# Kernel optimization log

Hardware: AMD Instinct MI355X
Metric: run time of the kernel (lower is better)

The kernel has to match this reference:

```python
import jax, jax.numpy as jnp
import numpy as np

N = 50000      # nodes
E = 800000     # edges (avg degree 16)
D_IN = 64
D_OUT = 64


def setup_inputs() -> dict:
    key = jax.random.key(0)
    k1, k2, k3 = jax.random.split(key, 3)
    x = jax.random.normal(k1, (N, D_IN), dtype=jnp.float32)
    edge_index = jax.random.randint(k2, (2, E), 0, N, dtype=jnp.int32)
    W = jax.random.normal(k3, (D_OUT, D_IN), dtype=jnp.float32) * 0.05
    b = jnp.zeros((D_OUT,), dtype=jnp.float32)
    prelu_a = jnp.full((1,), 0.25, dtype=jnp.float32)  # nn.PReLU() default
    return {"x": x, "edge_index": edge_index, "W": W, "b": b, "prelu_a": prelu_a}


def reference(x, edge_index, W, b, prelu_a):
    # GCNConv (PyG, normalize=True, add_self_loops=True) + PReLU.
    # Dropout is identity at inference and omitted.
    n = x.shape[0]
    row, col = edge_index[0], edge_index[1]
    loop = jnp.arange(n, dtype=edge_index.dtype)
    row = jnp.concatenate([row, loop])  # [E+N] source nodes
    col = jnp.concatenate([col, loop])  # [E+N] target nodes

    # Symmetric degree normalization: deg over targets (edge weight = 1).
    ones = jnp.ones(row.shape[0], dtype=x.dtype)
    deg = jax.ops.segment_sum(ones, col, num_segments=n)          # [N]
    dinv = jnp.where(deg > 0, jax.lax.rsqrt(deg), 0.0)            # deg^{-1/2}
    norm = dinv[row] * dinv[col]                                  # [E+N]

    h = x @ W.T                                                   # [N, D_OUT]
    msg = h[row] * norm[:, None]                                  # gather + scale
    out = jax.ops.segment_sum(msg, col, num_segments=n) + b       # scatter-add

    # PReLU with a single shared slope parameter
    return jnp.where(out >= 0, out, prelu_a * out)
```

## Files before the change

kernel.cpp:

```cpp
#include <hip/hip_runtime.h>
#include <hip/hip_bf16.h>

#define D 64
#define CAP 64
#define GROUPS 8
#define ZERO_BLOCKS 49

__global__ void __launch_bounds__(256) gemm_zero_kernel(
    const float* __restrict__ x, const float* __restrict__ W,
    __hip_bfloat16* __restrict__ h, int4* __restrict__ cnt4, int nzero4, int n)
{
    if (blockIdx.x < ZERO_BLOCKS) {
        int i = blockIdx.x * 256 + threadIdx.x;
        if (i < nzero4) cnt4[i] = make_int4(0, 0, 0, 0);
    }

    __shared__ float Ws[D * 65];
    __shared__ float xs[4][D];

    int tid = threadIdx.x;
    #pragma unroll
    for (int k = 0; k < 16; ++k) {
        int idx = tid + k * 256;
        int o = idx >> 6, i = idx & 63;
        Ws[o * 65 + i] = W[idx];
    }

    int ln = tid >> 6;
    int o  = tid & 63;
    int node = blockIdx.x * 4 + ln;
    if (node < n) {
        xs[ln][o] = x[node * D + o];
    }
    __syncthreads();

    if (node >= n) return;

    float sum = 0.0f;
    #pragma unroll
    for (int i = 0; i < D; ++i) {
        sum += xs[ln][i] * Ws[o * 65 + i];
    }
    h[(size_t)node * D + o] = __float2bfloat16(sum);
}

__global__ void __launch_bounds__(256) fill_kernel(
    const int* __restrict__ row, const int* __restrict__ col,
    const int4* __restrict__ row4, const int4* __restrict__ col4,
    int* __restrict__ cnt, unsigned short* __restrict__ srcs,
    int* __restrict__ ovf_cnt, int2* __restrict__ ovf, int E, int E4, int n)
{
    int g   = blockIdx.x & (GROUPS - 1);
    int bg  = blockIdx.x >> 3;
    int bpg = gridDim.x >> 3;
    int npg = (n + GROUPS - 1) / GROUPS;
    int lo  = g * npg;
    int hi  = lo + npg < n ? lo + npg : n;
    int stride = bpg * 256;

    for (int i = bg * 256 + threadIdx.x; i < E4; i += stride) {
        int4 cc = col4[i];
        int4 rr = row4[i];
        #pragma unroll
        for (int j = 0; j < 4; ++j) {
            int c = (j == 0) ? cc.x : (j == 1) ? cc.y : (j == 2) ? cc.z : cc.w;
            int r = (j == 0) ? rr.x : (j == 1) ? rr.y : (j == 2) ? rr.z : rr.w;
            if (c >= lo && c < hi) {
                int slot = atomicAdd(&cnt[c], 1);
                if (slot < CAP) {
                    srcs[(size_t)c * CAP + slot] = (unsigned short)r;
                } else {
                    int oi = atomicAdd(ovf_cnt, 1);
                    ovf[oi] = make_int2(r, c);
                }
            }
        }
    }
    for (int e = E4 * 4 + bg * 256 + threadIdx.x; e < E; e += stride) {
        int c = col[e];
        if (c >= lo && c < hi) {
            int r = row[e];
            int slot = atomicAdd(&cnt[c], 1);
            if (slot < CAP) {
                srcs[(size_t)c * CAP + slot] = (unsigned short)r;
            } else {
                int oi = atomicAdd(ovf_cnt, 1);
                ovf[oi] = make_int2(r, c);
            }
        }
    }
}

__global__ void __launch_bounds__(256) gather_kernel(
    const int* __restrict__ cnt, const unsigned short* __restrict__ srcs,
    const __hip_bfloat16* __restrict__ h,
    const float* __restrict__ b, const float* __restrict__ prelu_a,
    const int* __restrict__ ovf_cnt, const int2* __restrict__ ovf,
    float* __restrict__ out, int n)
{
    int wave = (blockIdx.x * blockDim.x + threadIdx.x) >> 6;
    int lane = threadIdx.x & 63;
    if (wave >= n) return;
    int c = wave;

    int deg = cnt[c];
    int m = deg < CAP ? deg : CAP;
    float dc = rsqrtf((float)deg + 1.0f);

    int   s  = 0;
    float wl = 0.0f;
    if (lane < m) {
        s  = (int)srcs[(size_t)c * CAP + lane];
        wl = rsqrtf((float)cnt[s] + 1.0f) * dc;
    }

    float acc = __bfloat162float(h[(size_t)c * D + lane]) * dc * dc + b[lane];

    int m8 = (m + 7) & ~7;
    for (int k = 0; k < m8; k += 8) {
        int   ss[8];
        float ww[8];
        #pragma unroll
        for (int j = 0; j < 8; ++j) {
            ss[j] = __shfl(s,  k + j);
            ww[j] = __shfl(wl, k + j);
        }
        float vv[8];
        #pragma unroll
        for (int j = 0; j < 8; ++j) {
            vv[j] = __bfloat162float(h[(size_t)ss[j] * D + lane]);
        }
        #pragma unroll
        for (int j = 0; j < 8; ++j) {
            acc += vv[j] * ww[j];
        }
    }

    int nov = *ovf_cnt;
    for (int i = 0; i < nov; ++i) {
        int2 rc = ovf[i];
        if (rc.y == c) {
            acc += __bfloat162float(h[(size_t)rc.x * D + lane]) *
                   rsqrtf((float)cnt[rc.x] + 1.0f) * dc;
        }
    }

    float al = prelu_a[0];
    out[(size_t)c * D + lane] = acc >= 0.0f ? acc : al * acc;
}

extern "C" void kernel_launch(void* const* d_in, const int* in_sizes, int n_in,
                              void* d_out, int out_size, void* d_ws, size_t ws_size,
                              hipStream_t stream) {
    const float* x       = (const float*)d_in[0];
    const int*   eidx    = (const int*)d_in[1];
    const float* W       = (const float*)d_in[2];
    const float* b       = (const float*)d_in[3];
    const float* prelu_a = (const float*)d_in[4];

    const int E = in_sizes[1] / 2;
    const int n = in_sizes[0] / D;
    const int* row = eidx;
    const int* col = eidx + E;

    float* out = (float*)d_out;

    int E4 = 0;
    if ((E % 4) == 0 &&
        ((uintptr_t)row % 16) == 0 && ((uintptr_t)col % 16) == 0) {
        E4 = E / 4;
    }

    int*   cnt     = (int*)d_ws;
    int*   ovf_cnt = cnt + n;
    int2*  ovf     = (int2*)(cnt + n + 2);
    __hip_bfloat16* h = (__hip_bfloat16*)(ovf + E);
    unsigned short* srcs = (unsigned short*)(h + (size_t)n * D);

    int nzero4 = (n + 1 + 3) / 4;

    gemm_zero_kernel<<<(n + 3) / 4, 256, 0, stream>>>(
        x, W, h, (int4*)cnt, nzero4, n);

    fill_kernel<<<2048, 256, 0, stream>>>(
        row, col, (const int4*)row, (const int4*)col,
        cnt, srcs, ovf_cnt, ovf, E, E4, n);

    gather_kernel<<<(n * 64 + 255) / 256, 256, 0, stream>>>(
        cnt, srcs, h, b, prelu_a, ovf_cnt, ovf, out, n);
}
```

Before: 100.2 us.

## Split feature dimension into two 32-channel halves with separate gather passes

The GEMM now writes h in a column-split layout: two contiguous [n,32] bf16 halves. The gather runs twice, once per half. Each half-wave handles alternate neighbors over 32 channels, and the two partial sums are combined with a cross-half shuffle. The goal is to shrink the working set of each gather pass so the random neighbor reads hit L2/MALL more often. The cost is a second launch and repeated reads of the CSR indices and degrees.

New measurement: 112.2 us. 1.12x slower.

```diff
diff --git a/kernel.cpp b/kernel.cpp
--- a/kernel.cpp
+++ b/kernel.cpp
@@ -41,7 +41,8 @@
     for (int i = 0; i < D; ++i) {
         sum += xs[ln][i] * Ws[o * 65 + i];
     }
-    h[(size_t)node * D + o] = __float2bfloat16(sum);
+    h[(size_t)(o >> 5) * n * 32 + (size_t)node * 32 + (o & 31)] =
+        __float2bfloat16(sum);
 }
 
 __global__ void __launch_bounds__(256) fill_kernel(
@@ -91,17 +92,19 @@
     }
 }
 
-__global__ void __launch_bounds__(256) gather_kernel(
+__global__ void __launch_bounds__(256) gather_half_kernel(
     const int* __restrict__ cnt, const unsigned short* __restrict__ srcs,
-    const __hip_bfloat16* __restrict__ h,
+    const __hip_bfloat16* __restrict__ hh,
     const float* __restrict__ b, const float* __restrict__ prelu_a,
     const int* __restrict__ ovf_cnt, const int2* __restrict__ ovf,
-    float* __restrict__ out, int n)
+    float* __restrict__ out, int n, int half)
 {
     int wave = (blockIdx.x * blockDim.x + threadIdx.x) >> 6;
     int lane = threadIdx.x & 63;
     if (wave >= n) return;
-    int c = wave;
+    int c  = wave;
+    int p  = lane >> 5;
+    int ch = lane & 31;
 
     int deg = cnt[c];
     int m = deg < CAP ? deg : CAP;
@@ -114,39 +117,45 @@
         wl = rsqrtf((float)cnt[s] + 1.0f) * dc;
     }
 
-    float acc = __bfloat162float(h[(size_t)c * D + lane]) * dc * dc + b[lane];
-
+    float acc = 0.0f;
     int m8 = (m + 7) & ~7;
     for (int k = 0; k < m8; k += 8) {
-        int   ss[8];
-        float ww[8];
-        #pragma unroll
-        for (int j = 0; j < 8; ++j) {
-            ss[j] = __shfl(s,  k + j);
-            ww[j] = __shfl(wl, k + j);
-        }
-        float vv[8];
-        #pragma unroll
-        for (int j = 0; j < 8; ++j) {
-            vv[j] = __bfloat162float(h[(size_t)ss[j] * D + lane]);
-        }
-        #pragma unroll
-        for (int j = 0; j < 8; ++j) {
-            acc += vv[j] * ww[j];
-        }
-    }
+        int   s4[4];
+        float w4[4];
+        #pragma unroll
+        for (int jj = 0; jj < 4; ++jj) {
+            s4[jj] = __shfl(s,  k + 2 * jj + p);
+            w4[jj] = __shfl(wl, k + 2 * jj + p);
+        }
+        float v4[4];
+        #pragma unroll
+        for (int jj = 0; jj < 4; ++jj) {
+            v4[jj] = __bfloat162float(hh[((size_t)s4[jj] << 5) + ch]);
+        }
+        #pragma unroll
+        for (int jj = 0; jj < 4; ++jj) {
+            acc += v4[jj] * w4[jj];
+        }
+    }
+
+    acc += __shfl_xor(acc, 32);
+
+    acc += __bfloat162float(hh[((size_t)c << 5) + ch]) * dc * dc + b[half * 32 + ch];
 
     int nov = *ovf_cnt;
     for (int i = 0; i < nov; ++i) {
         int2 rc = ovf[i];
         if (rc.y == c) {
-            acc += __bfloat162float(h[(size_t)rc.x * D + lane]) *
+            acc += __bfloat162float(hh[((size_t)rc.x << 5) + ch]) *
                    rsqrtf((float)cnt[rc.x] + 1.0f) * dc;
         }
     }
 
     float al = prelu_a[0];
-    out[(size_t)c * D + lane] = acc >= 0.0f ? acc : al * acc;
+    acc = acc >= 0.0f ? acc : al * acc;
+    if (p == 0) {
+        out[(size_t)c * D + half * 32 + ch] = acc;
+    }
 }
 
 extern "C" void kernel_launch(void* const* d_in, const int* in_sizes, int n_in,
@@ -175,7 +184,7 @@
     int*   ovf_cnt = cnt + n;
     int2*  ovf     = (int2*)(cnt + n + 2);
     __hip_bfloat16* h = (__hip_bfloat16*)(ovf + E);
-    unsigned short* srcs = (unsigned short*)(h + (size_t)n * D);
+    unsigned short* srcs = (unsigned short*)(h + (size_t)2 * n * 32);
 
     int nzero4 = (n + 1 + 3) / 4;
 
@@ -186,6 +195,9 @@
         row, col, (const int4*)row, (const int4*)col,
         cnt, srcs, ovf_cnt, ovf, E, E4, n);
 
-    gather_kernel<<<(n * 64 + 255) / 256, 256, 0, stream>>>(
-        cnt, srcs, h, b, prelu_a, ovf_cnt, ovf, out, n);
-}
+    int gblocks = (n * 64 + 255) / 256;
+    gather_half_kernel<<<gblocks, 256, 0, stream>>>(
+        cnt, srcs, h, b, prelu_a, ovf_cnt, ovf, out, n, 0);
+    gather_half_kernel<<<gblocks, 256, 0, stream>>>(
+        cnt, srcs, h + (size_t)n * 32, b, prelu_a, ovf_cnt, ovf, out, n, 1);
+}
```
